# Performance work log

Hardware: AMD Instinct MI355X
Metric: run time of the kernel (lower is better)

## Reference

```python
import jax, jax.numpy as jnp
import numpy as np

N_NODES = 20000
N_EDGES = 200000
N_GRAPHS = 128
IN_DIM = 256
HID = 512
HEADS = 8
C = HID // HEADS  # 64
LAT = 256
NEG_SLOPE = 0.2
BN_EPS = 1e-5


def setup_inputs() -> dict:
    key = jax.random.key(0)
    ks = jax.random.split(key, 24)
    n = lambda k, s, sc=0.05: jax.random.normal(k, s, jnp.float32) * sc
    return {
        'x': jax.random.normal(ks[0], (N_NODES, IN_DIM), jnp.float32),
        'edge_index': jax.random.randint(ks[1], (2, N_EDGES), 0, N_NODES, jnp.int32),
        'batch': jnp.sort(jax.random.randint(ks[2], (N_NODES,), 0, N_GRAPHS, jnp.int32)),
        'Wl0': n(ks[3], (IN_DIM, HID)), 'bl0': n(ks[4], (HID,)),
        'Wr0': n(ks[5], (IN_DIM, HID)), 'br0': n(ks[6], (HID,)),
        'att0': n(ks[7], (HEADS, C)), 'bias0': n(ks[8], (HID,)),
        'Wl1': n(ks[9], (HID, HID)), 'bl1': n(ks[10], (HID,)),
        'Wr1': n(ks[11], (HID, HID)), 'br1': n(ks[12], (HID,)),
        'att1': n(ks[13], (HEADS, C)), 'bias1': n(ks[14], (HID,)),
        'bn_gamma': jnp.ones((HID,), jnp.float32),
        'bn_beta': jnp.zeros((HID,), jnp.float32),
        'bn_mean': n(ks[15], (HID,)),
        'bn_var': jax.random.uniform(ks[16], (HID,), jnp.float32, 0.5, 1.5),
        'Wfc': n(ks[17], (HID, LAT)), 'bfc': n(ks[18], (LAT,)),
    }


def gatv2_layer(x, src, dst, Wl, bl, Wr, br, att, bias):
    # x: [N, F]; returns [N, HEADS*C]. GATv2: e = a . LeakyReLU(Wl x_src + Wr x_dst)
    xl = (x @ Wl + bl).reshape(-1, HEADS, C)  # source transform [N,H,C]
    xr = (x @ Wr + br).reshape(-1, HEADS, C)  # target transform [N,H,C]
    feat = jax.nn.leaky_relu(xl[src] + xr[dst], NEG_SLOPE)     # [E,H,C]
    logits = jnp.einsum('ehc,hc->eh', feat, att)               # [E,H]
    # segment softmax over incoming edges of each target node
    m = jax.ops.segment_max(logits, dst, num_segments=N_NODES)  # [N,H]
    p = jnp.exp(logits - m[dst])
    denom = jax.ops.segment_sum(p, dst, num_segments=N_NODES)   # [N,H]
    alpha = p / (denom[dst] + 1e-16)                            # [E,H]
    msg = xl[src] * alpha[:, :, None]                           # [E,H,C]
    out = jax.ops.segment_sum(msg, dst, num_segments=N_NODES)   # [N,H,C]
    return out.reshape(-1, HEADS * C) + bias


def reference(x, edge_index, batch, Wl0, bl0, Wr0, br0, att0, bias0,
              Wl1, bl1, Wr1, br1, att1, bias1,
              bn_gamma, bn_beta, bn_mean, bn_var, Wfc, bfc):
    src, dst = edge_index[0], edge_index[1]
    # layer 0 + ELU (dropout is identity in eval mode)
    h = jax.nn.elu(gatv2_layer(x, src, dst, Wl0, bl0, Wr0, br0, att0, bias0))
    # layer 1 + ELU
    h = jax.nn.elu(gatv2_layer(h, src, dst, Wl1, bl1, Wr1, br1, att1, bias1))
    # global add pool over graphs
    g = jax.ops.segment_sum(h, batch, num_segments=N_GRAPHS)  # [G, HID]
    # BatchNorm1d (eval mode: running stats)
    g = (g - bn_mean) * jax.lax.rsqrt(bn_var + BN_EPS) * bn_gamma + bn_beta
    return g @ Wfc + bfc  # [G, LAT]
```

## Files before the change

### kernel.cpp

```cpp
#include <hip/hip_runtime.h>
#include <hip/hip_bf16.h>
#include <cstdint>

#define NN 20000
#define NE 200000
#define NG 128
#define HID 512
#define XLR_W 1024

typedef __attribute__((ext_vector_type(4))) float f32x4;
typedef __attribute__((ext_vector_type(8))) short s16x8;

__device__ __forceinline__ float bf2f(unsigned short u) {
  union { unsigned int i; float f; } v; v.i = ((unsigned int)u) << 16; return v.f;
}
__device__ __forceinline__ unsigned short f2bf(float f) {
  union { float f; unsigned int i; } v; v.f = f;
  unsigned int i = v.i + 0x7FFFu + ((v.i >> 16) & 1u);
  return (unsigned short)(i >> 16);
}
__device__ __forceinline__ float asf(unsigned int u) {
  union { unsigned int i; float f; } v; v.i = u; return v.f;
}

#define GLOAD16(gp, lp)                                                        \
  __builtin_amdgcn_global_load_lds(                                            \
      (const __attribute__((address_space(1))) unsigned int*)(gp),             \
      (__attribute__((address_space(3))) unsigned int*)(lp), 16, 0, 0)

__global__ __launch_bounds__(256) void k_prep(const float* __restrict__ x,
                                              unsigned short* __restrict__ xb,
                                              const float* __restrict__ Wl0, const float* __restrict__ bl0,
                                              const float* __restrict__ Wr0, const float* __restrict__ br0,
                                              unsigned short* __restrict__ wt0, float* __restrict__ bcat0,
                                              const float* __restrict__ Wl1, const float* __restrict__ bl1,
                                              const float* __restrict__ Wr1, const float* __restrict__ br1,
                                              unsigned short* __restrict__ wt1, float* __restrict__ bcat1,
                                              int* __restrict__ deg) {
  int b = blockIdx.x, t = threadIdx.x;
  if (b < 79) {
    int i = b * 256 + t;
    if (i < NN) deg[i] = 0;
  } else if (b < 5079) {
    int i = (b - 79) * 256 + t;
    float4 v = ((const float4*)x)[i];
    ushort4 o;
    o.x = f2bf(v.x); o.y = f2bf(v.y); o.z = f2bf(v.z); o.w = f2bf(v.w);
    ((ushort4*)xb)[i] = o;
  } else if (b < 6103) {
    int id = (b - 5079) * 256 + t;
    int nrow = id >> 8, k = id & 255;
    float v = (nrow < HID) ? Wl0[k * HID + nrow] : Wr0[k * HID + (nrow - HID)];
    wt0[id] = f2bf(v);
    if (id < XLR_W) bcat0[id] = (id < HID) ? bl0[id] : br0[id - HID];
  } else {
    int id = (b - 6103) * 256 + t;
    int nrow = id >> 9, k = id & 511;
    float v = (nrow < HID) ? Wl1[k * HID + nrow] : Wr1[k * HID + (nrow - HID)];
    wt1[id] = f2bf(v);
    if (id < XLR_W) bcat1[id] = (id < HID) ? bl1[id] : br1[id - HID];
  }
}

__global__ void k_hist(const int* __restrict__ dst, int* __restrict__ deg, int E) {
  int i = blockIdx.x * blockDim.x + threadIdx.x;
  if (i < E) atomicAdd(&deg[dst[i]], 1);
}

__global__ __launch_bounds__(1024) void k_scan1(const int* __restrict__ deg,
                                                int* __restrict__ offs,
                                                int* __restrict__ btot, int n) {
  __shared__ int wsum[16];
  int t = threadIdx.x;
  int wid = t >> 6, lane = t & 63;
  int i = blockIdx.x * 1024 + t;
  int v = (i < n) ? deg[i] : 0;
  int s = v;
#pragma unroll
  for (int off = 1; off < 64; off <<= 1) {
    int x = __shfl_up(s, off, 64);
    if (lane >= off) s += x;
  }
  if (lane == 63) wsum[wid] = s;
  __syncthreads();
  if (wid == 0) {
    int ws = (lane < 16) ? wsum[lane] : 0;
#pragma unroll
    for (int off = 1; off < 16; off <<= 1) {
      int x = __shfl_up(ws, off, 64);
      if (lane >= off) ws += x;
    }
    if (lane < 16) wsum[lane] = ws;
  }
  __syncthreads();
  int ex = s - v + (wid ? wsum[wid - 1] : 0);
  if (i < n) offs[i] = ex;
  if (t == 1023) btot[blockIdx.x] = ex + v;
}

__global__ __launch_bounds__(1024) void k_scan3(int* __restrict__ offs,
                                                const int* __restrict__ btot,
                                                int* __restrict__ woff, int n, int nb) {
  __shared__ int sbofs;
  int t = threadIdx.x;
  if (t < 64) {
    int v = (t < nb) ? btot[t] : 0;
    int s = v;
#pragma unroll
    for (int off = 1; off < 64; off <<= 1) {
      int x = __shfl_up(s, off, 64);
      if (t >= off) s += x;
    }
    if (t == (int)blockIdx.x) sbofs = s - v;
    if (blockIdx.x == (unsigned)(nb - 1) && t == nb - 1) offs[n] = s;
  }
  __syncthreads();
  int add = sbofs;
  int i = blockIdx.x * 1024 + t;
  if (i < n) {
    int v = offs[i] + add;
    offs[i] = v;
    woff[i] = v;
  }
}

__global__ void k_scatter(const int* __restrict__ src, const int* __restrict__ dst,
                          int* __restrict__ woff, int* __restrict__ src_s, int E) {
  int i = blockIdx.x * blockDim.x + threadIdx.x;
  if (i < E) {
    int d = dst[i];
    int pos = atomicAdd(&woff[d], 1);
    src_s[pos] = src[i];
  }
}

#define BM 128
#define BN 128
#define BK 32

__global__ __launch_bounds__(256) void k_gemm(const unsigned short* __restrict__ A,
                                              const unsigned short* __restrict__ Bt,
                                              const float* __restrict__ bias,
                                              unsigned short* __restrict__ C,
                                              int M, int N, int K) {
  __shared__ __align__(16) unsigned short As[2][BM * BK];
  __shared__ __align__(16) unsigned short Bs[2][BN * BK];
  int m0 = blockIdx.y * BM, n0 = blockIdx.x * BN;
  int t = threadIdx.x;
  int wave = t >> 6, lane = t & 63;
  int wm = (wave >> 1) * 64, wn = (wave & 1) * 64;
  int ml = lane & 15, mq = lane >> 4;
  int lr = lane >> 2;
  int lc = (lane & 3) * 8;

  f32x4 acc[4][4];
#pragma unroll
  for (int i = 0; i < 4; i++)
#pragma unroll
    for (int j = 0; j < 4; j++) acc[i][j] = (f32x4)0.0f;

  int ar0 = m0 + wave * 32 + lr;      if (ar0 > M - 1) ar0 = M - 1;
  int ar1 = m0 + wave * 32 + 16 + lr; if (ar1 > M - 1) ar1 = M - 1;
  const unsigned short* ga0 = A + (size_t)ar0 * K + lc;
  const unsigned short* ga1 = A + (size_t)ar1 * K + lc;
  const unsigned short* gb0 = Bt + (size_t)(n0 + wave * 32 + lr) * K + lc;
  const unsigned short* gb1 = gb0 + (size_t)16 * K;
  int lo0 = (wave * 32) * BK;
  int lo1 = (wave * 32 + 16) * BK;

  GLOAD16(ga0, &As[0][lo0]);
  GLOAD16(ga1, &As[0][lo1]);
  GLOAD16(gb0, &Bs[0][lo0]);
  GLOAD16(gb1, &Bs[0][lo1]);
  ga0 += BK; ga1 += BK; gb0 += BK; gb1 += BK;

  int T = K / BK;
  for (int tt = 0; tt < T; tt++) {
    int cur = tt & 1, nxt = cur ^ 1;
    __syncthreads();
    if (tt + 1 < T) {
      GLOAD16(ga0, &As[nxt][lo0]);
      GLOAD16(ga1, &As[nxt][lo1]);
      GLOAD16(gb0, &Bs[nxt][lo0]);
      GLOAD16(gb1, &Bs[nxt][lo1]);
      ga0 += BK; ga1 += BK; gb0 += BK; gb1 += BK;
    }
    s16x8 af[4], bfr[4];
#pragma unroll
    for (int i = 0; i < 4; i++)
      af[i] = *(const s16x8*)(&As[cur][(wm + i * 16 + ml) * BK + mq * 8]);
#pragma unroll
    for (int j = 0; j < 4; j++)
      bfr[j] = *(const s16x8*)(&Bs[cur][(wn + j * 16 + ml) * BK + mq * 8]);
#pragma unroll
    for (int i = 0; i < 4; i++)
#pragma unroll
      for (int j = 0; j < 4; j++)
        acc[i][j] = __builtin_amdgcn_mfma_f32_16x16x32_bf16(af[i], bfr[j], acc[i][j], 0, 0, 0);
  }

#pragma unroll
  for (int i = 0; i < 4; i++) {
#pragma unroll
    for (int j = 0; j < 4; j++) {
      int col = n0 + wn + j * 16 + ml;
      float bcol = bias[col];
#pragma unroll
      for (int r = 0; r < 4; r++) {
        int row = m0 + wm + i * 16 + mq * 4 + r;
        if (row < M) C[(size_t)row * N + col] = f2bf(acc[i][j][r] + bcol);
      }
    }
  }
}

__global__ __launch_bounds__(256) void k_attn(const unsigned short* __restrict__ xlr,
                                              const float* __restrict__ att,
                                              const int* __restrict__ offs,
                                              const int* __restrict__ src_s,
                                              const float* __restrict__ bias,
                                              unsigned short* __restrict__ hout) {
  __shared__ float red[4][8][68];
  __shared__ float reds[4][8];
  int n = blockIdx.x;
  int wave = threadIdx.x >> 6, lane = threadIdx.x & 63;
  int h = lane >> 3, k = lane & 7;
  int c = h * 64 + k * 8;
  int s0 = offs[n], s1 = offs[n + 1];

  uint4 uxr = *(const uint4*)(xlr + (size_t)n * XLR_W + HID + c);
  float xr[8];
  xr[0] = asf(uxr.x << 16); xr[1] = asf(uxr.x & 0xFFFF0000u);
  xr[2] = asf(uxr.y << 16); xr[3] = asf(uxr.y & 0xFFFF0000u);
  xr[4] = asf(uxr.z << 16); xr[5] = asf(uxr.z & 0xFFFF0000u);
  xr[6] = asf(uxr.w << 16); xr[7] = asf(uxr.w & 0xFFFF0000u);
  float at[8];
  {
    const float4* ap = (const float4*)(att + c);
    float4 a0 = ap[0], a1 = ap[1];
    at[0] = a0.x; at[1] = a0.y; at[2] = a0.z; at[3] = a0.w;
    at[4] = a1.x; at[5] = a1.y; at[6] = a1.z; at[7] = a1.w;
  }

  float acc[8] = {0.f, 0.f, 0.f, 0.f, 0.f, 0.f, 0.f, 0.f};
  float sum = 0.0f;

  int i = s0 + wave;
  uint4 u_cur = make_uint4(0, 0, 0, 0);
  if (i < s1) {
    int s = src_s[i];
    u_cur = *(const uint4*)(xlr + (size_t)s * XLR_W + c);
  }
  int nx = i + 4;
  for (; i < s1; i += 4) {
    uint4 u = u_cur;
    if (nx < s1) {
      int s = src_s[nx];
      u_cur = *(const uint4*)(xlr + (size_t)s * XLR_W + c);
    }
    nx += 4;

    float xl[8];
    xl[0] = asf(u.x << 16); xl[1] = asf(u.x & 0xFFFF0000u);
    xl[2] = asf(u.y << 16); xl[3] = asf(u.y & 0xFFFF0000u);
    xl[4] = asf(u.z << 16); xl[5] = asf(u.z & 0xFFFF0000u);
    xl[6] = asf(u.w << 16); xl[7] = asf(u.w & 0xFFFF0000u);

    float l = 0.0f;
#pragma unroll
    for (int j = 0; j < 8; j++) {
      float v = xl[j] + xr[j];
      v = fmaf(0.4f, fabsf(v), 0.6f * v);
      l = fmaf(v, at[j], l);
    }
    l += __shfl_xor(l, 1, 64);
    l += __shfl_xor(l, 2, 64);
    l += __shfl_xor(l, 4, 64);

    float p = __expf(l);
    sum += p;
#pragma unroll
    for (int j = 0; j < 8; j++) acc[j] = fmaf(p, xl[j], acc[j]);
  }

#pragma unroll
  for (int j = 0; j < 8; j++) red[wave][h][k * 8 + j] = acc[j];
  if (k == 0) reds[wave][h] = sum;
  __syncthreads();

  int t = threadIdx.x;
  int cc = t * 2;
  int hh = cc >> 6, off = cc & 63;
  float a0 = red[0][hh][off] + red[1][hh][off] + red[2][hh][off] + red[3][hh][off];
  float a1 = red[0][hh][off + 1] + red[1][hh][off + 1] + red[2][hh][off + 1] + red[3][hh][off + 1];
  float sm = reds[0][hh] + reds[1][hh] + reds[2][hh] + reds[3][hh];
  float di = 1.0f / (sm + 1e-16f);
  float o_a = a0 * di + bias[cc];
  float o_b = a1 * di + bias[cc + 1];
  o_a = o_a > 0.0f ? o_a : (__expf(o_a) - 1.0f);
  o_b = o_b > 0.0f ? o_b : (__expf(o_b) - 1.0f);
  unsigned int up = (unsigned int)f2bf(o_a) | ((unsigned int)f2bf(o_b) << 16);
  *(unsigned int*)(hout + (size_t)n * HID + cc) = up;
}

__device__ __forceinline__ int lower_bound(const int* __restrict__ a, int n, int key) {
  int lo = 0, hi = n;
  while (lo < hi) { int mid = (lo + hi) >> 1; if (a[mid] < key) lo = mid + 1; else hi = mid; }
  return lo;
}

__global__ __launch_bounds__(256) void k_pool(const unsigned short* __restrict__ h,
                                              const int* __restrict__ batch,
                                              float* __restrict__ part) {
  int g = blockIdx.x, p = blockIdx.y, t = threadIdx.x;
  int start = lower_bound(batch, NN, g);
  int end = lower_bound(batch, NN, g + 1);
  int cntq = (end - start + 3) >> 2;
  int lo = start + p * cntq;
  int hi = lo + cntq; if (hi > end) hi = end;
  int c = t * 2;
  float a0 = 0.0f, a1 = 0.0f;
  for (int n = lo; n < hi; n++) {
    unsigned int u = *(const unsigned int*)(h + (size_t)n * HID + c);
    a0 += asf(u << 16);
    a1 += asf(u & 0xFFFF0000u);
  }
  float* dstp = part + ((size_t)g * 4 + p) * HID + c;
  dstp[0] = a0;
  dstp[1] = a1;
}

__global__ __launch_bounds__(256) void k_fc(const float* __restrict__ part,
                                            const float* __restrict__ gamma,
                                            const float* __restrict__ beta,
                                            const float* __restrict__ mean,
                                            const float* __restrict__ var,
                                            const float* __restrict__ Wfc,
                                            const float* __restrict__ bfc,
                                            float* __restrict__ out) {
  __shared__ float xsm[512];
  int g = blockIdx.x, t = threadIdx.x;
  for (int c = t; c < HID; c += 256) {
    float s = part[((size_t)g * 4 + 0) * HID + c] + part[((size_t)g * 4 + 1) * HID + c]
            + part[((size_t)g * 4 + 2) * HID + c] + part[((size_t)g * 4 + 3) * HID + c];
    xsm[c] = (s - mean[c]) * rsqrtf(var[c] + 1e-5f) * gamma[c] + beta[c];
  }
  __syncthreads();
  float acc = bfc[t];
#pragma unroll 8
  for (int k = 0; k < 512; k++) acc += xsm[k] * Wfc[k * 256 + t];
  out[g * 256 + t] = acc;
}

extern "C" void kernel_launch(void* const* d_in, const int* in_sizes, int n_in,
                              void* d_out, int out_size, void* d_ws, size_t ws_size,
                              hipStream_t stream) {
  const float* x     = (const float*)d_in[0];
  const int* ei      = (const int*)d_in[1];
  const int* batch   = (const int*)d_in[2];
  const float* Wl0   = (const float*)d_in[3];
  const float* bl0   = (const float*)d_in[4];
  const float* Wr0   = (const float*)d_in[5];
  const float* br0   = (const float*)d_in[6];
  const float* att0  = (const float*)d_in[7];
  const float* bias0 = (const float*)d_in[8];
  const float* Wl1   = (const float*)d_in[9];
  const float* bl1   = (const float*)d_in[10];
  const float* Wr1   = (const float*)d_in[11];
  const float* br1   = (const float*)d_in[12];
  const float* att1  = (const float*)d_in[13];
  const float* bias1 = (const float*)d_in[14];
  const float* gamma = (const float*)d_in[15];
  const float* beta  = (const float*)d_in[16];
  const float* mean  = (const float*)d_in[17];
  const float* var   = (const float*)d_in[18];
  const float* Wfc   = (const float*)d_in[19];
  const float* bfc   = (const float*)d_in[20];

  const int* src = ei;
  const int* dst = ei + NE;

  char* w = (char*)d_ws;
  size_t off = 0;
  auto alloc = [&](size_t bytes) -> void* {
    void* p = w + off;
    off += (bytes + 255) & ~(size_t)255;
    return p;
  };
  int* deg            = (int*)alloc((size_t)NN * 4);
  int* offs           = (int*)alloc((size_t)(NN + 1) * 4);
  int* woff           = (int*)alloc((size_t)NN * 4);
  int* src_s          = (int*)alloc((size_t)NE * 4);
  int* btot           = (int*)alloc((size_t)32 * 4);
  unsigned short* xb  = (unsigned short*)alloc((size_t)NN * 256 * 2);
  unsigned short* xlr = (unsigned short*)alloc((size_t)NN * XLR_W * 2);
  unsigned short* hb  = (unsigned short*)alloc((size_t)NN * HID * 2);
  unsigned short* wt0 = (unsigned short*)alloc((size_t)XLR_W * 256 * 2);
  unsigned short* wt1 = (unsigned short*)alloc((size_t)XLR_W * HID * 2);
  float* bcat0        = (float*)alloc((size_t)XLR_W * 4);
  float* bcat1        = (float*)alloc((size_t)XLR_W * 4);
  float* part         = (float*)alloc((size_t)NG * 4 * HID * 4);

  const int NB = (NN + 1023) / 1024;

  k_prep<<<8151, 256, 0, stream>>>(x, xb, Wl0, bl0, Wr0, br0, wt0, bcat0,
                                   Wl1, bl1, Wr1, br1, wt1, bcat1, deg);
  k_hist<<<(NE + 255) / 256, 256, 0, stream>>>(dst, deg, NE);
  k_scan1<<<NB, 1024, 0, stream>>>(deg, offs, btot, NN);
  k_scan3<<<NB, 1024, 0, stream>>>(offs, btot, woff, NN, NB);
  k_scatter<<<(NE + 255) / 256, 256, 0, stream>>>(src, dst, woff, src_s, NE);

  k_gemm<<<dim3(XLR_W / BN, (NN + BM - 1) / BM), 256, 0, stream>>>(xb, wt0, bcat0, xlr, NN, XLR_W, 256);
  k_attn<<<NN, 256, 0, stream>>>(xlr, att0, offs, src_s, bias0, hb);

  k_gemm<<<dim3(XLR_W / BN, (NN + BM - 1) / BM), 256, 0, stream>>>(hb, wt1, bcat1, xlr, NN, XLR_W, 512);
  k_attn<<<NN, 256, 0, stream>>>(xlr, att1, offs, src_s, bias1, hb);

  k_pool<<<dim3(NG, 4), 256, 0, stream>>>(hb, batch, part);
  k_fc<<<NG, 256, 0, stream>>>(part, gamma, beta, mean, var, Wfc, bfc, (float*)d_out);
}
```

Before: 340.5 us.

## Replace LDS-tiled GEMM with per-wave register-direct MFMA tiles

The GEMM drops shared-memory staging and block-level syncs. Each wave now owns an independent 64x64 output tile and loads its A/B fragments straight from global memory into registers, with a one-step register prefetch. This removes LDS traffic and __syncthreads, but the four waves no longer share operand tiles, so global/L2 reads for A and B rise and reuse depends on cache hits.

```diff
diff --git a/kernel.cpp b/kernel.cpp
--- a/kernel.cpp
+++ b/kernel.cpp
@@ -22,11 +22,6 @@
 __device__ __forceinline__ float asf(unsigned int u) {
   union { unsigned int i; float f; } v; v.i = u; return v.f;
 }
-
-#define GLOAD16(gp, lp)                                                        \
-  __builtin_amdgcn_global_load_lds(                                            \
-      (const __attribute__((address_space(1))) unsigned int*)(gp),             \
-      (__attribute__((address_space(3))) unsigned int*)(lp), 16, 0, 0)
 
 __global__ __launch_bounds__(256) void k_prep(const float* __restrict__ x,
                                               unsigned short* __restrict__ xb,
@@ -134,24 +129,29 @@
   }
 }
 
-#define BM 128
-#define BN 128
-#define BK 32
-
 __global__ __launch_bounds__(256) void k_gemm(const unsigned short* __restrict__ A,
                                               const unsigned short* __restrict__ Bt,
                                               const float* __restrict__ bias,
                                               unsigned short* __restrict__ C,
                                               int M, int N, int K) {
-  __shared__ __align__(16) unsigned short As[2][BM * BK];
-  __shared__ __align__(16) unsigned short Bs[2][BN * BK];
-  int m0 = blockIdx.y * BM, n0 = blockIdx.x * BN;
   int t = threadIdx.x;
   int wave = t >> 6, lane = t & 63;
-  int wm = (wave >> 1) * 64, wn = (wave & 1) * 64;
+  int wid = blockIdx.x * 4 + wave;
+  int mi = wid >> 4, ni = wid & 15;
+  int m0 = mi * 64, n0 = ni * 64;
+  if (m0 >= M) return;
   int ml = lane & 15, mq = lane >> 4;
-  int lr = lane >> 2;
-  int lc = (lane & 3) * 8;
+
+  const unsigned short* pa[4];
+  const unsigned short* pb[4];
+#pragma unroll
+  for (int i = 0; i < 4; i++) {
+    int row = m0 + i * 16 + ml; if (row > M - 1) row = M - 1;
+    pa[i] = A + (size_t)row * K + mq * 8;
+  }
+#pragma unroll
+  for (int j = 0; j < 4; j++)
+    pb[j] = Bt + (size_t)(n0 + j * 16 + ml) * K + mq * 8;
 
   f32x4 acc[4][4];
 #pragma unroll
@@ -159,55 +159,43 @@
 #pragma unroll
     for (int j = 0; j < 4; j++) acc[i][j] = (f32x4)0.0f;
 
-  int ar0 = m0 + wave * 32 + lr;      if (ar0 > M - 1) ar0 = M - 1;
-  int ar1 = m0 + wave * 32 + 16 + lr; if (ar1 > M - 1) ar1 = M - 1;
-  const unsigned short* ga0 = A + (size_t)ar0 * K + lc;
-  const unsigned short* ga1 = A + (size_t)ar1 * K + lc;
-  const unsigned short* gb0 = Bt + (size_t)(n0 + wave * 32 + lr) * K + lc;
-  const unsigned short* gb1 = gb0 + (size_t)16 * K;
-  int lo0 = (wave * 32) * BK;
-  int lo1 = (wave * 32 + 16) * BK;
-
-  GLOAD16(ga0, &As[0][lo0]);
-  GLOAD16(ga1, &As[0][lo1]);
-  GLOAD16(gb0, &Bs[0][lo0]);
-  GLOAD16(gb1, &Bs[0][lo1]);
-  ga0 += BK; ga1 += BK; gb0 += BK; gb1 += BK;
-
-  int T = K / BK;
-  for (int tt = 0; tt < T; tt++) {
-    int cur = tt & 1, nxt = cur ^ 1;
-    __syncthreads();
-    if (tt + 1 < T) {
-      GLOAD16(ga0, &As[nxt][lo0]);
-      GLOAD16(ga1, &As[nxt][lo1]);
-      GLOAD16(gb0, &Bs[nxt][lo0]);
-      GLOAD16(gb1, &Bs[nxt][lo1]);
-      ga0 += BK; ga1 += BK; gb0 += BK; gb1 += BK;
-    }
-    s16x8 af[4], bfr[4];
+  s16x8 ac[4], bc[4], an[4], bn[4];
+#pragma unroll
+  for (int i = 0; i < 4; i++) { ac[i] = *(const s16x8*)pa[i]; pa[i] += 32; }
+#pragma unroll
+  for (int j = 0; j < 4; j++) { bc[j] = *(const s16x8*)pb[j]; pb[j] += 32; }
+
+  int T = K >> 5;
+  for (int tt = 0; tt < T - 1; tt++) {
+#pragma unroll
+    for (int i = 0; i < 4; i++) { an[i] = *(const s16x8*)pa[i]; pa[i] += 32; }
+#pragma unroll
+    for (int j = 0; j < 4; j++) { bn[j] = *(const s16x8*)pb[j]; pb[j] += 32; }
 #pragma unroll
     for (int i = 0; i < 4; i++)
-      af[i] = *(const s16x8*)(&As[cur][(wm + i * 16 + ml) * BK + mq * 8]);
+#pragma unroll
+      for (int j = 0; j < 4; j++)
+        acc[i][j] = __builtin_amdgcn_mfma_f32_16x16x32_bf16(ac[i], bc[j], acc[i][j], 0, 0, 0);
+#pragma unroll
+    for (int i = 0; i < 4; i++) ac[i] = an[i];
+#pragma unroll
+    for (int j = 0; j < 4; j++) bc[j] = bn[j];
+  }
+#pragma unroll
+  for (int i = 0; i < 4; i++)
 #pragma unroll
     for (int j = 0; j < 4; j++)
-      bfr[j] = *(const s16x8*)(&Bs[cur][(wn + j * 16 + ml) * BK + mq * 8]);
-#pragma unroll
-    for (int i = 0; i < 4; i++)
-#pragma unroll
-      for (int j = 0; j < 4; j++)
-        acc[i][j] = __builtin_amdgcn_mfma_f32_16x16x32_bf16(af[i], bfr[j], acc[i][j], 0, 0, 0);
-  }
+      acc[i][j] = __builtin_amdgcn_mfma_f32_16x16x32_bf16(ac[i], bc[j], acc[i][j], 0, 0, 0);
 
 #pragma unroll
   for (int i = 0; i < 4; i++) {
 #pragma unroll
     for (int j = 0; j < 4; j++) {
-      int col = n0 + wn + j * 16 + ml;
+      int col = n0 + j * 16 + ml;
       float bcol = bias[col];
 #pragma unroll
       for (int r = 0; r < 4; r++) {
-        int row = m0 + wm + i * 16 + mq * 4 + r;
+        int row = m0 + i * 16 + mq * 4 + r;
         if (row < M) C[(size_t)row * N + col] = f2bf(acc[i][j][r] + bcol);
       }
     }
@@ -410,10 +398,12 @@
   k_scan3<<<NB, 1024, 0, stream>>>(offs, btot, woff, NN, NB);
   k_scatter<<<(NE + 255) / 256, 256, 0, stream>>>(src, dst, woff, src_s, NE);
 
-  k_gemm<<<dim3(XLR_W / BN, (NN + BM - 1) / BM), 256, 0, stream>>>(xb, wt0, bcat0, xlr, NN, XLR_W, 256);
+  const int GB = ((NN + 63) / 64) * 16 / 4;
+
+  k_gemm<<<GB, 256, 0, stream>>>(xb, wt0, bcat0, xlr, NN, XLR_W, 256);
   k_attn<<<NN, 256, 0, stream>>>(xlr, att0, offs, src_s, bias0, hb);
 
-  k_gemm<<<dim3(XLR_W / BN, (NN + BM - 1) / BM), 256, 0, stream>>>(hb, wt1, bcat1, xlr, NN, XLR_W, 512);
+  k_gemm<<<GB, 256, 0, stream>>>(hb, wt1, bcat1, xlr, NN, XLR_W, 512);
   k_attn<<<NN, 256, 0, stream>>>(xlr, att1, offs, src_s, bias1, hb);
 
   k_pool<<<dim3(NG, 4), 256, 0, stream>>>(hb, batch, part);
```

Result: slower. 386.1 us (+13.4%).

## Use single-buffered K=64 tiles in GEMM instead of double-buffered K=32

Applied to the files above, without the earlier changes.

The GEMM kernel now loads a K=64 slab per iteration as two 32-wide planes into shared memory, then runs two MFMA sub-steps on it. The double-buffered prefetch is removed, so each iteration issues its loads, syncs, computes, and syncs again. This halves the number of loop iterations and barriers per unit of K. The cost is that global-to-LDS loads no longer overlap the MFMA work of the previous tile.

```diff
diff --git a/kernel.cpp b/kernel.cpp
--- a/kernel.cpp
+++ b/kernel.cpp
@@ -136,22 +136,22 @@
 
 #define BM 128
 #define BN 128
-#define BK 32
+#define PLN 4096
 
 __global__ __launch_bounds__(256) void k_gemm(const unsigned short* __restrict__ A,
                                               const unsigned short* __restrict__ Bt,
                                               const float* __restrict__ bias,
                                               unsigned short* __restrict__ C,
                                               int M, int N, int K) {
-  __shared__ __align__(16) unsigned short As[2][BM * BK];
-  __shared__ __align__(16) unsigned short Bs[2][BN * BK];
+  __shared__ __align__(16) unsigned short As[2 * PLN];
+  __shared__ __align__(16) unsigned short Bs[2 * PLN];
   int m0 = blockIdx.y * BM, n0 = blockIdx.x * BN;
   int t = threadIdx.x;
   int wave = t >> 6, lane = t & 63;
   int wm = (wave >> 1) * 64, wn = (wave & 1) * 64;
   int ml = lane & 15, mq = lane >> 4;
   int lr = lane >> 2;
-  int lc = (lane & 3) * 8;
+  int lq = (lane & 3) * 8;
 
   f32x4 acc[4][4];
 #pragma unroll
@@ -159,44 +159,47 @@
 #pragma unroll
     for (int j = 0; j < 4; j++) acc[i][j] = (f32x4)0.0f;
 
-  int ar0 = m0 + wave * 32 + lr;      if (ar0 > M - 1) ar0 = M - 1;
-  int ar1 = m0 + wave * 32 + 16 + lr; if (ar1 > M - 1) ar1 = M - 1;
-  const unsigned short* ga0 = A + (size_t)ar0 * K + lc;
-  const unsigned short* ga1 = A + (size_t)ar1 * K + lc;
-  const unsigned short* gb0 = Bt + (size_t)(n0 + wave * 32 + lr) * K + lc;
-  const unsigned short* gb1 = gb0 + (size_t)16 * K;
-  int lo0 = (wave * 32) * BK;
-  int lo1 = (wave * 32 + 16) * BK;
-
-  GLOAD16(ga0, &As[0][lo0]);
-  GLOAD16(ga1, &As[0][lo1]);
-  GLOAD16(gb0, &Bs[0][lo0]);
-  GLOAD16(gb1, &Bs[0][lo1]);
-  ga0 += BK; ga1 += BK; gb0 += BK; gb1 += BK;
-
-  int T = K / BK;
+  const unsigned short* gA[4];
+  const unsigned short* gB[4];
+  unsigned short* lA[4];
+  unsigned short* lB[4];
+#pragma unroll
+  for (int p = 0; p < 2; p++)
+#pragma unroll
+    for (int h = 0; h < 2; h++) {
+      int idx = p * 2 + h;
+      int arow = m0 + wave * 32 + h * 16 + lr; if (arow > M - 1) arow = M - 1;
+      gA[idx] = A + (size_t)arow * K + p * 32 + lq;
+      gB[idx] = Bt + (size_t)(n0 + wave * 32 + h * 16 + lr) * K + p * 32 + lq;
+      lA[idx] = &As[p * PLN + (wave * 32 + h * 16) * 32];
+      lB[idx] = &Bs[p * PLN + (wave * 32 + h * 16) * 32];
+    }
+
+  int T = K >> 6;
   for (int tt = 0; tt < T; tt++) {
-    int cur = tt & 1, nxt = cur ^ 1;
+#pragma unroll
+    for (int idx = 0; idx < 4; idx++) {
+      GLOAD16(gA[idx], lA[idx]);
+      GLOAD16(gB[idx], lB[idx]);
+      gA[idx] += 64; gB[idx] += 64;
+    }
     __syncthreads();
-    if (tt + 1 < T) {
-      GLOAD16(ga0, &As[nxt][lo0]);
-      GLOAD16(ga1, &As[nxt][lo1]);
-      GLOAD16(gb0, &Bs[nxt][lo0]);
-      GLOAD16(gb1, &Bs[nxt][lo1]);
-      ga0 += BK; ga1 += BK; gb0 += BK; gb1 += BK;
-    }
-    s16x8 af[4], bfr[4];
-#pragma unroll
-    for (int i = 0; i < 4; i++)
-      af[i] = *(const s16x8*)(&As[cur][(wm + i * 16 + ml) * BK + mq * 8]);
-#pragma unroll
-    for (int j = 0; j < 4; j++)
-      bfr[j] = *(const s16x8*)(&Bs[cur][(wn + j * 16 + ml) * BK + mq * 8]);
-#pragma unroll
-    for (int i = 0; i < 4; i++)
+#pragma unroll
+    for (int kq = 0; kq < 2; kq++) {
+      s16x8 af[4], bfr[4];
+#pragma unroll
+      for (int i = 0; i < 4; i++)
+        af[i] = *(const s16x8*)(&As[kq * PLN + (wm + i * 16 + ml) * 32 + mq * 8]);
 #pragma unroll
       for (int j = 0; j < 4; j++)
-        acc[i][j] = __builtin_amdgcn_mfma_f32_16x16x32_bf16(af[i], bfr[j], acc[i][j], 0, 0, 0);
+        bfr[j] = *(const s16x8*)(&Bs[kq * PLN + (wn + j * 16 + ml) * 32 + mq * 8]);
+#pragma unroll
+      for (int i = 0; i < 4; i++)
+#pragma unroll
+        for (int j = 0; j < 4; j++)
+          acc[i][j] = __builtin_amdgcn_mfma_f32_16x16x32_bf16(af[i], bfr[j], acc[i][j], 0, 0, 0);
+    }
+    __syncthreads();
   }
 
 #pragma unroll
```

Result: faster. 324.9 us (-4.6%).
